# Kernel optimization log

Hardware: AMD Instinct MI355X
Metric: run time of the kernel (lower is better)

Reference implementation:

```python
import jax, jax.numpy as jnp
import numpy as np


def _normalized_histograms(x, num_bins):
    # x: (B, C, H, W) in [0, 1]. Returns (B*C, num_bins) normalized histograms.
    B, C, H, W = x.shape
    rows = B * C
    flat = x.reshape(rows, H * W)
    # torch.histc semantics on [0,1]: bin i covers [i/nb, (i+1)/nb), last bin
    # also includes 1.0 -> floor(x*nb) clipped to [0, nb-1].
    idx = jnp.clip(jnp.floor(flat * num_bins).astype(jnp.int32), 0, num_bins - 1)
    # Offset each (b,c) row into its own segment range, one segment_sum for all.
    seg = (idx + jnp.arange(rows, dtype=jnp.int32)[:, None] * num_bins).reshape(-1)
    counts = jax.ops.segment_sum(
        jnp.ones(seg.shape, dtype=x.dtype), seg, num_segments=rows * num_bins
    ).reshape(rows, num_bins)
    return counts / counts.sum(axis=1, keepdims=True)


def setup_inputs() -> dict:
    key = jax.random.key(0)
    k1, k2 = jax.random.split(key)
    B, C, H, W = 16, 3, 1024, 1024
    output = jax.random.uniform(k1, (B, C, H, W), dtype=jnp.float32)
    target = jax.random.uniform(k2, (B, C, H, W), dtype=jnp.float32)
    return {"output": output, "target": target, "num_bins": 256}


def reference(output, target, num_bins):
    h_out = _normalized_histograms(output, num_bins)
    h_tgt = _normalized_histograms(target, num_bins)
    # sum over (b,c) of mean-over-bins L1, divided by B*C == global mean.
    return jnp.abs(h_out - h_tgt).mean()
```

## Files before the change

### kernel.cpp

```cpp
#include <hip/hip_runtime.h>


#define NB    256
#define HW_N  (1024 * 1024)
#define ROWS  48
#define BLOCKS_PER_ROW 32
#define THREADS 256


__global__ __launch_bounds__(THREADS) void hist_kernel(
    const float* __restrict__ out_t,
    const float* __restrict__ tgt_t,
    unsigned int* __restrict__ counts)
{
    __shared__ unsigned int lh[NB];
    const int tid = threadIdx.x;
    for (int i = tid; i < NB; i += THREADS) lh[i] = 0u;
    __syncthreads();

    const int blk = blockIdx.x;
    const int seg = blk / BLOCKS_PER_ROW;
    const int sub = blk % BLOCKS_PER_ROW;
    const float* src = (seg < ROWS) ? out_t : tgt_t;
    const int row = (seg < ROWS) ? seg : (seg - ROWS);

    const size_t base = (size_t)row * HW_N + (size_t)sub * (HW_N / BLOCKS_PER_ROW);
    const float4* __restrict__ p = reinterpret_cast<const float4*>(src + base);
    const int n4 = HW_N / BLOCKS_PER_ROW / 4;

    for (int i = tid; i < n4; i += THREADS) {
        float4 v = p[i];
        int i0 = min(max((int)floorf(v.x * (float)NB), 0), NB - 1);
        int i1 = min(max((int)floorf(v.y * (float)NB), 0), NB - 1);
        int i2 = min(max((int)floorf(v.z * (float)NB), 0), NB - 1);
        int i3 = min(max((int)floorf(v.w * (float)NB), 0), NB - 1);
        atomicAdd(&lh[i0], 1u);
        atomicAdd(&lh[i1], 1u);
        atomicAdd(&lh[i2], 1u);
        atomicAdd(&lh[i3], 1u);
    }
    __syncthreads();

    unsigned int* __restrict__ g = counts + (size_t)seg * NB;
    for (int i = tid; i < NB; i += THREADS) {
        unsigned int c = lh[i];
        if (c) atomicAdd(&g[i], c);
    }
}

__global__ __launch_bounds__(THREADS) void reduce_kernel(
    const unsigned int* __restrict__ counts,
    float* __restrict__ out)
{
    const int tid = threadIdx.x;
    long long acc = 0;
    for (int r = 0; r < ROWS; ++r) {
        int a = (int)counts[(size_t)r * NB + tid];
        int b = (int)counts[(size_t)(ROWS + r) * NB + tid];
        int d = a - b;
        acc += (long long)((d < 0) ? -d : d);
    }
    __shared__ long long s[THREADS];
    s[tid] = acc;
    __syncthreads();
    for (int off = THREADS / 2; off >= 1; off >>= 1) {
        if (tid < off) s[tid] += s[tid + off];
        __syncthreads();
    }
    if (tid == 0) {
        double v = (double)s[0] / ((double)HW_N * (double)ROWS * (double)NB);
        out[0] = (float)v;
    }
}

extern "C" void kernel_launch(void* const* d_in, const int* in_sizes, int n_in,
                              void* d_out, int out_size, void* d_ws, size_t ws_size,
                              hipStream_t stream) {
    const float* out_t = (const float*)d_in[0];
    const float* tgt_t = (const float*)d_in[1];
    unsigned int* counts = (unsigned int*)d_ws;
    float* out = (float*)d_out;

    const size_t counts_bytes = (size_t)2 * ROWS * NB * sizeof(unsigned int);
    hipMemsetAsync(counts, 0, counts_bytes, stream);

    dim3 grid(2 * ROWS * BLOCKS_PER_ROW);
    dim3 block(THREADS);
    hist_kernel<<<grid, block, 0, stream>>>(out_t, tgt_t, counts);
    reduce_kernel<<<1, block, 0, stream>>>(counts, out);
}
```

Measured before the change: 399.8 us.

## Use per-wave shared histograms and block partials instead of global atomics

Each block now keeps one shared-memory histogram per wavefront, which spreads LDS atomic contention across four copies. Blocks write their partial histograms straight to workspace instead of issuing global atomics. A per-row kernel then sums the partials and takes the L1 difference, and a tiny kernel finalizes the mean. The grid is halved to 16 blocks per row with a manually unrolled load loop of four float4s per iteration, which adds an extra kernel launch and partial-buffer traffic.

New measurement: 395.9 us. No clear change (-1.0%).

```diff
diff --git a/kernel.cpp b/kernel.cpp
--- a/kernel.cpp
+++ b/kernel.cpp
@@ -1,76 +1,97 @@
 #include <hip/hip_runtime.h>
 
 
-#define NB    256
-#define HW_N  (1024 * 1024)
-#define ROWS  48
-#define BLOCKS_PER_ROW 32
-#define THREADS 256
+#define NB       256
+#define HW_N     (1024 * 1024)
+#define ROWS     48
+#define SEGS     (2 * ROWS)
+#define SUBS     16
+#define THREADS  256
+#define NWAVES   (THREADS / 64)
 
 
 __global__ __launch_bounds__(THREADS) void hist_kernel(
     const float* __restrict__ out_t,
     const float* __restrict__ tgt_t,
-    unsigned int* __restrict__ counts)
+    unsigned int* __restrict__ partials)
 {
-    __shared__ unsigned int lh[NB];
+    __shared__ unsigned int lh[NWAVES][NB];
     const int tid = threadIdx.x;
-    for (int i = tid; i < NB; i += THREADS) lh[i] = 0u;
+    const int wid = tid >> 6;
+
+    #pragma unroll
+    for (int w = 0; w < NWAVES; ++w)
+        for (int i = tid; i < NB; i += THREADS) lh[w][i] = 0u;
     __syncthreads();
 
     const int blk = blockIdx.x;
-    const int seg = blk / BLOCKS_PER_ROW;
-    const int sub = blk % BLOCKS_PER_ROW;
+    const int seg = blk / SUBS;
+    const int sub = blk % SUBS;
     const float* src = (seg < ROWS) ? out_t : tgt_t;
     const int row = (seg < ROWS) ? seg : (seg - ROWS);
 
-    const size_t base = (size_t)row * HW_N + (size_t)sub * (HW_N / BLOCKS_PER_ROW);
+    const int elems = HW_N / SUBS;
+    const size_t base = (size_t)row * HW_N + (size_t)sub * elems;
     const float4* __restrict__ p = reinterpret_cast<const float4*>(src + base);
-    const int n4 = HW_N / BLOCKS_PER_ROW / 4;
 
-    for (int i = tid; i < n4; i += THREADS) {
-        float4 v = p[i];
-        int i0 = min(max((int)floorf(v.x * (float)NB), 0), NB - 1);
-        int i1 = min(max((int)floorf(v.y * (float)NB), 0), NB - 1);
-        int i2 = min(max((int)floorf(v.z * (float)NB), 0), NB - 1);
-        int i3 = min(max((int)floorf(v.w * (float)NB), 0), NB - 1);
-        atomicAdd(&lh[i0], 1u);
-        atomicAdd(&lh[i1], 1u);
-        atomicAdd(&lh[i2], 1u);
-        atomicAdd(&lh[i3], 1u);
+    unsigned int* __restrict__ h = lh[wid];
+    for (int t = 0; t < 16; ++t) {
+        const int i0 = t * 1024 + tid;
+        float4 a = p[i0];
+        float4 b = p[i0 + 256];
+        float4 c = p[i0 + 512];
+        float4 d = p[i0 + 768];
+        #define BIN(x) min(max((int)floorf((x) * (float)NB), 0), NB - 1)
+        atomicAdd(&h[BIN(a.x)], 1u); atomicAdd(&h[BIN(a.y)], 1u);
+        atomicAdd(&h[BIN(a.z)], 1u); atomicAdd(&h[BIN(a.w)], 1u);
+        atomicAdd(&h[BIN(b.x)], 1u); atomicAdd(&h[BIN(b.y)], 1u);
+        atomicAdd(&h[BIN(b.z)], 1u); atomicAdd(&h[BIN(b.w)], 1u);
+        atomicAdd(&h[BIN(c.x)], 1u); atomicAdd(&h[BIN(c.y)], 1u);
+        atomicAdd(&h[BIN(c.z)], 1u); atomicAdd(&h[BIN(c.w)], 1u);
+        atomicAdd(&h[BIN(d.x)], 1u); atomicAdd(&h[BIN(d.y)], 1u);
+        atomicAdd(&h[BIN(d.z)], 1u); atomicAdd(&h[BIN(d.w)], 1u);
+        #undef BIN
     }
     __syncthreads();
 
-    unsigned int* __restrict__ g = counts + (size_t)seg * NB;
+    unsigned int* __restrict__ g = partials + (size_t)blk * NB;
     for (int i = tid; i < NB; i += THREADS) {
-        unsigned int c = lh[i];
-        if (c) atomicAdd(&g[i], c);
+        unsigned int c = lh[0][i] + lh[1][i] + lh[2][i] + lh[3][i];
+        g[i] = c;
     }
 }
 
-__global__ __launch_bounds__(THREADS) void reduce_kernel(
-    const unsigned int* __restrict__ counts,
-    float* __restrict__ out)
+__global__ __launch_bounds__(THREADS) void rowdiff_kernel(
+    const unsigned int* __restrict__ partials,
+    unsigned int* __restrict__ gsum)
 {
-    const int tid = threadIdx.x;
-    long long acc = 0;
-    for (int r = 0; r < ROWS; ++r) {
-        int a = (int)counts[(size_t)r * NB + tid];
-        int b = (int)counts[(size_t)(ROWS + r) * NB + tid];
-        int d = a - b;
-        acc += (long long)((d < 0) ? -d : d);
+    const int r = blockIdx.x;
+    const int bin = threadIdx.x;
+    unsigned int a = 0, b = 0;
+    #pragma unroll
+    for (int s = 0; s < SUBS; ++s) {
+        a += partials[((size_t)(r)         * SUBS + s) * NB + bin];
+        b += partials[((size_t)(ROWS + r)  * SUBS + s) * NB + bin];
     }
-    __shared__ long long s[THREADS];
-    s[tid] = acc;
+    int d = (int)a - (int)b;
+    unsigned int ad = (unsigned int)((d < 0) ? -d : d);
+
+    __shared__ unsigned int s[THREADS];
+    s[bin] = ad;
     __syncthreads();
     for (int off = THREADS / 2; off >= 1; off >>= 1) {
-        if (tid < off) s[tid] += s[tid + off];
+        if (bin < off) s[bin] += s[bin + off];
         __syncthreads();
     }
-    if (tid == 0) {
-        double v = (double)s[0] / ((double)HW_N * (double)ROWS * (double)NB);
-        out[0] = (float)v;
-    }
+    if (bin == 0) atomicAdd(gsum, s[0]);
+}
+
+__global__ void finalize_kernel(const unsigned int* __restrict__ gsum,
+                                float* __restrict__ out)
+{
+    double v = (double)(*gsum) /
+               ((double)HW_N * (double)ROWS * (double)NB);
+    out[0] = (float)v;
 }
 
 extern "C" void kernel_launch(void* const* d_in, const int* in_sizes, int n_in,
@@ -78,14 +99,13 @@
                               hipStream_t stream) {
     const float* out_t = (const float*)d_in[0];
     const float* tgt_t = (const float*)d_in[1];
-    unsigned int* counts = (unsigned int*)d_ws;
+    unsigned int* partials = (unsigned int*)d_ws;
+    unsigned int* gsum = partials + (size_t)SEGS * SUBS * NB;
     float* out = (float*)d_out;
 
-    const size_t counts_bytes = (size_t)2 * ROWS * NB * sizeof(unsigned int);
-    hipMemsetAsync(counts, 0, counts_bytes, stream);
+    hipMemsetAsync(gsum, 0, sizeof(unsigned int), stream);
 
-    dim3 grid(2 * ROWS * BLOCKS_PER_ROW);
-    dim3 block(THREADS);
-    hist_kernel<<<grid, block, 0, stream>>>(out_t, tgt_t, counts);
-    reduce_kernel<<<1, block, 0, stream>>>(counts, out);
+    hist_kernel<<<dim3(SEGS * SUBS), dim3(THREADS), 0, stream>>>(out_t, tgt_t, partials);
+    rowdiff_kernel<<<dim3(ROWS), dim3(THREADS), 0, stream>>>(partials, gsum);
+    finalize_kernel<<<1, 1, 0, stream>>>(gsum, out);
 }
```
